# Kernel optimization log

Hardware: AMD Instinct MI355X
Metric: run time of the kernel (lower is better)

The kernel has to match this reference:

```python
import jax, jax.numpy as jnp
import numpy as np

ALPHA = 0.5    # SpikeAct surrogate width (act_fun(alpha=0.5))
DECAY = 0.2    # membrane decay
THRESH = 0.5   # firing threshold (requires_grad=False -> constant)


@jax.custom_vjp
def spike_act(x):
    # Heaviside spike with rectangular surrogate gradient
    return (x > 0).astype(x.dtype)

def _sa_fwd(x):
    return spike_act(x), x

def _sa_bwd(x, g):
    return (g * (jnp.abs(x) < ALPHA).astype(g.dtype),)

spike_act.defvjp(_sa_fwd, _sa_bwd)


@jax.custom_vjp
def ei_act(x):
    # EI sign gate with straight-through gradient
    return jnp.sign(x)

def _ei_fwd(x):
    return ei_act(x), None

def _ei_bwd(_, g):
    return (g,)

ei_act.defvjp(_ei_fwd, _ei_bwd)


def conv2d(x, w, b):
    # x: [B,C,H,W], w: [O,I,kh,kw] (OIHW), SAME padding, stride 1
    y = jax.lax.conv_general_dilated(
        x, w, window_strides=(1, 1), padding='SAME',
        dimension_numbers=('NCHW', 'OIHW', 'NCHW'))
    return y + b[None, :, None, None]


def setup_inputs() -> dict:
    key = jax.random.key(0)
    k0, k1, k2 = jax.random.split(key, 3)
    T, B, C, H, W, K = 8, 16, 128, 32, 32, 5
    fan_in = C * K * K
    x = jax.random.normal(k0, (T, B, C, H, W), jnp.float32)
    back_w = jax.random.normal(k1, (C, C, K, K), jnp.float32) / np.float32(np.sqrt(fan_in))
    back_b = jnp.zeros((C,), jnp.float32)
    ei_w = jax.random.normal(k2, (C, C, K, K), jnp.float32) / np.float32(np.sqrt(fan_in))
    ei_b = jnp.zeros((C,), jnp.float32)
    return {"x": x, "back_w": back_w, "back_b": back_b, "ei_w": ei_w, "ei_b": ei_b}


def reference(x, back_w, back_b, ei_w, ei_b):
    # x: [T,B,C,H,W] -> spikes over time [T,B,C,H,W]
    state_shape = x.shape[1:]
    mem0 = jnp.zeros(state_shape, x.dtype)
    spike0 = jnp.zeros(state_shape, x.dtype)

    def step(carry, xt):
        mem, spike = carry
        # integral: decayed mem + feedback-conv sigmoid gate * input
        mem = DECAY * mem + jax.nn.sigmoid(conv2d(spike, back_w, back_b)) * xt
        # calc_spike (if_ei=True path)
        ei_gate = ei_act(conv2d(mem, ei_w, ei_b))
        s = spike_act(mem - THRESH)
        mem = mem * (1.0 - s)
        spike = ei_gate * s
        return (mem, spike), spike

    _, spikes = jax.lax.scan(step, (mem0, spike0), x)
    return spikes
```

## Files before the change

kernel.cpp:

```cpp
#include <hip/hip_runtime.h>
#include <math.h>

#define TDIM 512
#define CCH  128
#define HW   32
#define OCT  4
#define ICT  2
#define NPH  16
#define NTEAM 4
#define RPB  16
#define SW   36
#define SROWS 20
#define PLANE (SROWS * SW)

template<int EPI>
__global__ __launch_bounds__(TDIM, 8) void lif_conv(
    const float* __restrict__ cin,
    const float* __restrict__ wgt,
    const float* __restrict__ bias,
    const float* __restrict__ aux0,
    const float* __restrict__ aux1,
    float* __restrict__ out0,
    float* __restrict__ out1,
    int first)
{
    const int ocg  = blockIdx.x;
    const int half = blockIdx.y;
    const int b    = blockIdx.z;
    const int oc0  = ocg * OCT;
    const int r0   = half * RPB;
    const int tid  = threadIdx.x;
    const int team = tid >> 7;
    const int lt   = tid & 127;
    const int rl   = lt >> 3;
    const int cl   = (lt & 7) * 4;

    const int steam = __builtin_amdgcn_readfirstlane(team);

    __shared__ __align__(16) float s_in[NTEAM * ICT * PLANE];
    float* tin = s_in + team * (ICT * PLANE);

    float acc[OCT][4];
#pragma unroll
    for (int oc = 0; oc < OCT; ++oc)
#pragma unroll
        for (int j = 0; j < 4; ++j) acc[oc][j] = 0.f;

    if (!(EPI == 0 && first)) {
        const int icbase  = team * 32;
        const int sicbase = steam * 32;
        for (int i = tid; i < NTEAM * ICT * PLANE; i += TDIM) s_in[i] = 0.f;
        __syncthreads();

        for (int ph = 0; ph < NPH; ++ph) {
            for (int idx = lt; idx < ICT * SROWS * 8; idx += 128) {
                int p    = idx / (SROWS * 8);
                int rem  = idx - p * (SROWS * 8);
                int srow = rem >> 3;
                int sg   = rem & 7;
                int gr   = r0 + srow - 2;
                if (gr >= 0 && gr < HW) {
                    float4 v = *(const float4*)&cin[(((size_t)b * CCH + icbase + ph * ICT + p) * HW + gr) * HW + sg * 4];
                    float* dst = &tin[p * PLANE + srow * SW + 2 + sg * 4];
                    *(float2*)dst       = make_float2(v.x, v.y);
                    *(float2*)(dst + 2) = make_float2(v.z, v.w);
                }
            }
            __syncthreads();
#pragma unroll
            for (int ici = 0; ici < ICT; ++ici) {
                float win5[5][8];
#pragma unroll
                for (int kh = 0; kh < 5; ++kh) {
                    const float* src = &tin[ici * PLANE + (rl + kh) * SW + cl];
                    float4 a = *(const float4*)src;
                    float4 c = *(const float4*)(src + 4);
                    win5[kh][0] = a.x; win5[kh][1] = a.y; win5[kh][2] = a.z; win5[kh][3] = a.w;
                    win5[kh][4] = c.x; win5[kh][5] = c.y; win5[kh][6] = c.z; win5[kh][7] = c.w;
                }
                const float* wb = wgt + ((size_t)oc0 * CCH + sicbase + ph * ICT + ici) * 25;
#pragma unroll
                for (int oc = 0; oc < OCT; ++oc) {
                    const float* wo = wb + oc * (CCH * 25);
#pragma unroll
                    for (int kh = 0; kh < 5; ++kh) {
#pragma unroll
                        for (int kw = 0; kw < 5; ++kw) {
                            float wv = wo[kh * 5 + kw];
                            acc[oc][0] += win5[kh][kw]     * wv;
                            acc[oc][1] += win5[kh][kw + 1] * wv;
                            acc[oc][2] += win5[kh][kw + 2] * wv;
                            acc[oc][3] += win5[kh][kw + 3] * wv;
                        }
                    }
                }
            }
            __syncthreads();
        }

        float* red = s_in;
        if (team == 1)
#pragma unroll
            for (int oc = 0; oc < OCT; ++oc)
#pragma unroll
                for (int j = 0; j < 4; ++j) red[lt * 17 + oc * 4 + j] = acc[oc][j];
        if (team == 2)
#pragma unroll
            for (int oc = 0; oc < OCT; ++oc)
#pragma unroll
                for (int j = 0; j < 4; ++j) red[128 * 17 + lt * 17 + oc * 4 + j] = acc[oc][j];
        __syncthreads();
        if (team == 0)
#pragma unroll
            for (int oc = 0; oc < OCT; ++oc)
#pragma unroll
                for (int j = 0; j < 4; ++j)
                    acc[oc][j] += red[lt * 17 + oc * 4 + j] + red[128 * 17 + lt * 17 + oc * 4 + j];
        __syncthreads();
        if (team == 3)
#pragma unroll
            for (int oc = 0; oc < OCT; ++oc)
#pragma unroll
                for (int j = 0; j < 4; ++j) red[lt * 17 + oc * 4 + j] = acc[oc][j];
        __syncthreads();
        if (team == 0)
#pragma unroll
            for (int oc = 0; oc < OCT; ++oc)
#pragma unroll
                for (int j = 0; j < 4; ++j) acc[oc][j] += red[lt * 17 + oc * 4 + j];
    }

    if (team == 0) {
#pragma unroll
        for (int oc = 0; oc < OCT; ++oc) {
            const size_t pidx = (((size_t)b * CCH + oc0 + oc) * HW + (r0 + rl)) * HW + cl;
            const float bia = bias[oc0 + oc];
            float y[4];
#pragma unroll
            for (int j = 0; j < 4; ++j) y[j] = acc[oc][j] + bia;
            if (EPI == 0) {
                float4 xv = *(const float4*)(aux1 + pidx);
                float4 mv;
                if (first) { mv.x = mv.y = mv.z = mv.w = 0.f; }
                else       mv = *(const float4*)(aux0 + pidx);
                float4 mp;
                mp.x = 0.2f * mv.x + (1.f / (1.f + expf(-y[0]))) * xv.x;
                mp.y = 0.2f * mv.y + (1.f / (1.f + expf(-y[1]))) * xv.y;
                mp.z = 0.2f * mv.z + (1.f / (1.f + expf(-y[2]))) * xv.z;
                mp.w = 0.2f * mv.w + (1.f / (1.f + expf(-y[3]))) * xv.w;
                *(float4*)(out0 + pidx) = mp;
            } else {
                float4 m4 = *(const float4*)(aux0 + pidx);
                float g[4] = {
                    (y[0] > 0.f) ? 1.f : ((y[0] < 0.f) ? -1.f : 0.f),
                    (y[1] > 0.f) ? 1.f : ((y[1] < 0.f) ? -1.f : 0.f),
                    (y[2] > 0.f) ? 1.f : ((y[2] < 0.f) ? -1.f : 0.f),
                    (y[3] > 0.f) ? 1.f : ((y[3] < 0.f) ? -1.f : 0.f)};
                float m[4] = {m4.x, m4.y, m4.z, m4.w};
                float4 mn, sp;
                float s0 = (m[0] > 0.5f) ? 1.f : 0.f;
                float s1 = (m[1] > 0.5f) ? 1.f : 0.f;
                float s2 = (m[2] > 0.5f) ? 1.f : 0.f;
                float s3 = (m[3] > 0.5f) ? 1.f : 0.f;
                mn.x = m[0] * (1.f - s0); sp.x = g[0] * s0;
                mn.y = m[1] * (1.f - s1); sp.y = g[1] * s1;
                mn.z = m[2] * (1.f - s2); sp.z = g[2] * s2;
                mn.w = m[3] * (1.f - s3); sp.w = g[3] * s3;
                *(float4*)(out0 + pidx) = mn;
                *(float4*)(out1 + pidx) = sp;
            }
        }
    }
}

extern "C" void kernel_launch(void* const* d_in, const int* in_sizes, int n_in,
                              void* d_out, int out_size, void* d_ws, size_t ws_size,
                              hipStream_t stream) {
    const float* x      = (const float*)d_in[0];
    const float* back_w = (const float*)d_in[1];
    const float* back_b = (const float*)d_in[2];
    const float* ei_w   = (const float*)d_in[3];
    const float* ei_b   = (const float*)d_in[4];
    float* out = (float*)d_out;

    const size_t N = (size_t)16 * CCH * HW * HW;
    float* mem_cur  = (float*)d_ws;
    float* mem_post = mem_cur + N;

    dim3 grid(CCH / OCT, 2, 16);

    for (int t = 0; t < 8; ++t) {
        const float* spike_prev = (t == 0) ? x : (out + (size_t)(t - 1) * N);
        lif_conv<0><<<grid, TDIM, 0, stream>>>(
            spike_prev, back_w, back_b,
            mem_cur, x + (size_t)t * N,
            mem_post, nullptr, (t == 0) ? 1 : 0);
        lif_conv<1><<<grid, TDIM, 0, stream>>>(
            mem_post, ei_w, ei_b,
            mem_post, nullptr,
            mem_cur, out + (size_t)t * N, 0);
    }
}
```

Baseline: 2.369 ms.

## Give each wavefront a private LDS tile to drop block-wide barriers

Reorganizes the block so each of the 8 wavefronts owns an 8-row output strip and a private 12-row shared-memory input tile for its input-channel slice. This removes the two __syncthreads per input-channel phase, since each wave loads and consumes its own tile in order. The channel-split reduction is folded into a single store-then-sum step. The cost is more halo rows loaded per output row and a slightly larger shared-memory footprint.

```diff
diff --git a/kernel.cpp b/kernel.cpp
--- a/kernel.cpp
+++ b/kernel.cpp
@@ -7,11 +7,9 @@
 #define OCT  4
 #define ICT  2
 #define NPH  16
-#define NTEAM 4
-#define RPB  16
 #define SW   36
-#define SROWS 20
-#define PLANE (SROWS * SW)
+#define TROWS 12
+#define PLANE (TROWS * SW)
 
 template<int EPI>
 __global__ __launch_bounds__(TDIM, 8) void lif_conv(
@@ -28,17 +26,19 @@
     const int half = blockIdx.y;
     const int b    = blockIdx.z;
     const int oc0  = ocg * OCT;
-    const int r0   = half * RPB;
     const int tid  = threadIdx.x;
-    const int team = tid >> 7;
-    const int lt   = tid & 127;
-    const int rl   = lt >> 3;
-    const int cl   = (lt & 7) * 4;
+    const int w    = tid >> 6;
+    const int lane = tid & 63;
+    const int ks   = w >> 1;
+    const int rg   = w & 1;
+    const int r0   = half * 16 + rg * 8;
+    const int rl   = lane >> 3;
+    const int cl   = (lane & 7) * 4;
 
-    const int steam = __builtin_amdgcn_readfirstlane(team);
+    const int sks = __builtin_amdgcn_readfirstlane(ks);
 
-    __shared__ __align__(16) float s_in[NTEAM * ICT * PLANE];
-    float* tin = s_in + team * (ICT * PLANE);
+    __shared__ __align__(16) float s_in[8 * ICT * PLANE];
+    float* tin = s_in + w * (ICT * PLANE);
 
     float acc[OCT][4];
 #pragma unroll
@@ -47,26 +47,26 @@
         for (int j = 0; j < 4; ++j) acc[oc][j] = 0.f;
 
     if (!(EPI == 0 && first)) {
-        const int icbase  = team * 32;
-        const int sicbase = steam * 32;
-        for (int i = tid; i < NTEAM * ICT * PLANE; i += TDIM) s_in[i] = 0.f;
-        __syncthreads();
+        const int icbase = ks * 32;
+        const int sicb   = sks * 32;
+        for (int i = lane; i < ICT * PLANE; i += 64) tin[i] = 0.f;
 
         for (int ph = 0; ph < NPH; ++ph) {
-            for (int idx = lt; idx < ICT * SROWS * 8; idx += 128) {
-                int p    = idx / (SROWS * 8);
-                int rem  = idx - p * (SROWS * 8);
+#pragma unroll
+            for (int i = 0; i < 3; ++i) {
+                int idx  = i * 64 + lane;
+                int p    = (idx >= 96) ? 1 : 0;
+                int rem  = idx - p * 96;
                 int srow = rem >> 3;
                 int sg   = rem & 7;
                 int gr   = r0 + srow - 2;
-                if (gr >= 0 && gr < HW) {
+                if ((unsigned)gr < 32u) {
                     float4 v = *(const float4*)&cin[(((size_t)b * CCH + icbase + ph * ICT + p) * HW + gr) * HW + sg * 4];
                     float* dst = &tin[p * PLANE + srow * SW + 2 + sg * 4];
                     *(float2*)dst       = make_float2(v.x, v.y);
                     *(float2*)(dst + 2) = make_float2(v.z, v.w);
                 }
             }
-            __syncthreads();
 #pragma unroll
             for (int ici = 0; ici < ICT; ++ici) {
                 float win5[5][8];
@@ -78,7 +78,7 @@
                     win5[kh][0] = a.x; win5[kh][1] = a.y; win5[kh][2] = a.z; win5[kh][3] = a.w;
                     win5[kh][4] = c.x; win5[kh][5] = c.y; win5[kh][6] = c.z; win5[kh][7] = c.w;
                 }
-                const float* wb = wgt + ((size_t)oc0 * CCH + sicbase + ph * ICT + ici) * 25;
+                const float* wb = wgt + ((size_t)oc0 * CCH + sicb + ph * ICT + ici) * 25;
 #pragma unroll
                 for (int oc = 0; oc < OCT; ++oc) {
                     const float* wo = wb + oc * (CCH * 25);
@@ -95,42 +95,33 @@
                     }
                 }
             }
-            __syncthreads();
         }
 
+        __syncthreads();
         float* red = s_in;
-        if (team == 1)
-#pragma unroll
-            for (int oc = 0; oc < OCT; ++oc)
-#pragma unroll
-                for (int j = 0; j < 4; ++j) red[lt * 17 + oc * 4 + j] = acc[oc][j];
-        if (team == 2)
-#pragma unroll
-            for (int oc = 0; oc < OCT; ++oc)
-#pragma unroll
-                for (int j = 0; j < 4; ++j) red[128 * 17 + lt * 17 + oc * 4 + j] = acc[oc][j];
-        __syncthreads();
-        if (team == 0)
+        if (ks > 0) {
+            const int slot = ((ks - 1) * 128 + rg * 64 + lane) * 17;
 #pragma unroll
             for (int oc = 0; oc < OCT; ++oc)
 #pragma unroll
                 for (int j = 0; j < 4; ++j)
-                    acc[oc][j] += red[lt * 17 + oc * 4 + j] + red[128 * 17 + lt * 17 + oc * 4 + j];
+                    red[slot + oc * 4 + j] = acc[oc][j];
+        }
         __syncthreads();
-        if (team == 3)
+        if (ks == 0) {
 #pragma unroll
-            for (int oc = 0; oc < OCT; ++oc)
+            for (int q = 0; q < 3; ++q) {
+                const int slot = (q * 128 + rg * 64 + lane) * 17;
 #pragma unroll
-                for (int j = 0; j < 4; ++j) red[lt * 17 + oc * 4 + j] = acc[oc][j];
-        __syncthreads();
-        if (team == 0)
+                for (int oc = 0; oc < OCT; ++oc)
 #pragma unroll
-            for (int oc = 0; oc < OCT; ++oc)
-#pragma unroll
-                for (int j = 0; j < 4; ++j) acc[oc][j] += red[lt * 17 + oc * 4 + j];
+                    for (int j = 0; j < 4; ++j)
+                        acc[oc][j] += red[slot + oc * 4 + j];
+            }
+        }
     }
 
-    if (team == 0) {
+    if (ks == 0) {
 #pragma unroll
         for (int oc = 0; oc < OCT; ++oc) {
             const size_t pidx = (((size_t)b * CCH + oc0 + oc) * HW + (r0 + rl)) * HW + cl;
```

After: 2.461 ms. 3.9% more time.
